# Kernel tuning notes

Measured on AMD Instinct MI355X. Metric: run time of the kernel, lower is better.

Reference implementation:

```python
import jax, jax.numpy as jnp
import numpy as np

B, T, E, D, A, H, C, K = 32, 1500, 512, 512, 512, 4, 10, 201
SHARPENING = 1.0


def setup_inputs() -> dict:
    key = jax.random.key(0)
    ks = jax.random.split(key, 11)
    def w(k, shape, fan_in):
        return jax.random.normal(k, shape, jnp.float32) / np.sqrt(fan_in).astype(np.float32)
    return {
        "enc_out": jax.random.normal(ks[0], (B, T, E), jnp.float32),
        "x_lens": jax.random.randint(ks[1], (B,), T // 2, T + 1),
        "dec_out": jax.random.normal(ks[2], (B, 1, D), jnp.float32),
        # previous-step attention weights: a valid distribution over T per head
        "aw_step": jax.nn.softmax(jax.random.normal(ks[3], (B, T, H), jnp.float32), axis=1),
        "w_enc": w(ks[4], (H, E, A), E),   # per-head LinearND(enc->att)
        "b_enc": jnp.zeros((H, A), jnp.float32),
        "w_dec": w(ks[5], (H, D, A), D),   # per-head LinearND(dec->att), no bias
        "w_conv": w(ks[6], (H, C, A), C),  # per-head LinearND(conv_ch->att), no bias
        "conv_k": w(ks[7], (H * C, 1, K), K),  # grouped 1D conv kernels (O,I,K), groups=H
        "v": w(ks[8], (H, A), A),          # per-head LinearND(att->1), no bias
        "w_mha": w(ks[9], (H * E, E), H * E),
        "b_mha": jnp.zeros((E,), jnp.float32),
    }


def reference(enc_out, x_lens, dec_out, aw_step, w_enc, b_enc, w_dec, w_conv, conv_k, v, w_mha, b_mha):
    b, t, e = enc_out.shape
    h = aw_step.shape[-1]
    c = w_conv.shape[1]
    k = conv_k.shape[-1]
    # enc_out_a: per-head encoder projection [B,T,H,A]
    enc_a = jnp.einsum('bte,hea->btha', enc_out, w_enc) + b_enc
    # decoder projection, broadcast over time [B,1,H,A]
    dec_a = jnp.einsum('bd,hda->bha', dec_out[:, 0], w_dec)[:, None]
    # location features: grouped 1D conv over previous attention weights
    aw_t = jnp.transpose(aw_step, (0, 2, 1))  # [B,H,T]
    conv = jax.lax.conv_general_dilated(
        aw_t, conv_k, window_strides=(1,), padding=[(k // 2, k // 2)],
        dimension_numbers=('NCH', 'OIH', 'NCH'), feature_group_count=h)  # [B,H*C,T]
    conv = conv.reshape(b, h, c, t).transpose(0, 3, 1, 2)  # [B,T,H,C]
    conv_a = jnp.einsum('bthc,hca->btha', conv, w_conv)
    # additive energy [B,T,H]
    energy = jnp.einsum('btha,ha->bth', jnp.tanh(enc_a + dec_a + conv_a), v)
    # original code multiplies energy by mask (1 valid, -1024 padded) then sharpening
    mask = jnp.where(jnp.arange(t)[None, :] < x_lens[:, None], 1.0, -1024.0).astype(energy.dtype)
    energy = energy * mask[:, :, None] * SHARPENING
    aw = jax.nn.softmax(energy, axis=1)  # softmax over time per head
    # per-head context, concatenated along feature dim -> [B,1,H*E]
    ctx = jnp.einsum('bte,bth->bhe', enc_out, aw).reshape(b, 1, h * e)
    ctx = ctx @ w_mha + b_mha  # [B,1,E]
    return ctx, aw
```

## Files before the change

kernel.cpp:

```cpp
#include <hip/hip_runtime.h>
#include <hip/hip_bf16.h>

#define BB 32
#define TT 1500
#define TP 1536
#define EE 512
#define HH 4
#define AA 512
#define NN 2048
#define CC 10
#define KCONV 201
#define KAUG 576

typedef __attribute__((ext_vector_type(8))) __bf16 bf16x8;
typedef __attribute__((ext_vector_type(4))) float f32x4;

__device__ __forceinline__ unsigned short f2bf(float x) {
    unsigned int u = __float_as_uint(x);
    u = (u + 0x7fffu + ((u >> 16) & 1u)) >> 16;
    return (unsigned short)u;
}
__device__ __forceinline__ float bf2f(unsigned short u) {
    return __uint_as_float(((unsigned int)u) << 16);
}
__device__ __forceinline__ void glds16(const void* g, void* l) {
    __builtin_amdgcn_global_load_lds(
        (const __attribute__((address_space(1))) unsigned int*)g,
        (__attribute__((address_space(3))) unsigned int*)l, 16, 0, 0);
}
__device__ __forceinline__ float tanh_fast(float x) {
    float e = __expf(x * 2.0f);
    return fmaf(-2.0f, __builtin_amdgcn_rcpf(e + 1.0f), 1.0f);
}

#define PREP_DEC0   0
#define PREP_CONV0  32
#define PREP_WT0    7712
#define PREP_PAD0   12320
#define PREP_ENC0   19412
#define PREP_TOTAL  43412

__global__ __launch_bounds__(256) void k_prep(
    const float* __restrict__ enc, const int* __restrict__ xl,
    const float* __restrict__ dec_out, const float* __restrict__ aw_step,
    const float* __restrict__ w_enc, const float* __restrict__ b_enc,
    const float* __restrict__ w_dec, const float* __restrict__ w_conv,
    const float* __restrict__ conv_k,
    unsigned short* __restrict__ Whi, unsigned short* __restrict__ Wlo,
    unsigned short* __restrict__ Ahi, unsigned short* __restrict__ Alo,
    float* __restrict__ dec_a) {
    __shared__ float sbuf[456 + KCONV];
    const int bid = blockIdx.x;
    const int tid = threadIdx.x;

    if (bid < PREP_CONV0) {
        const int h = bid >> 3;
        const int a = ((bid & 7) << 6) + (tid & 63);
        const int bg = tid >> 6;
        float acc[8] = {0.f, 0.f, 0.f, 0.f, 0.f, 0.f, 0.f, 0.f};
        const float* wp = w_dec + (size_t)h * 512 * 512 + a;
#pragma unroll 4
        for (int d = 0; d < 512; ++d) {
            float w = wp[(size_t)d * 512];
#pragma unroll
            for (int q = 0; q < 8; ++q)
                acc[q] += dec_out[(size_t)(bg * 8 + q) * 512 + d] * w;
        }
        const float be = b_enc[h * 512 + a];
#pragma unroll
        for (int q = 0; q < 8; ++q)
            dec_a[(size_t)(bg * 8 + q) * NN + h * 512 + a] = be + acc[q];
    } else if (bid < PREP_WT0) {
        int r = bid - PREP_CONV0;
        const int tch = r % 6;
        const int hc  = (r / 6) % 40;
        const int b   = r / 240;
        const int h   = hc / 10;
        const int t0  = tch * 256;
        float* sAw = sbuf;
        float* sK  = sbuf + 456;
        for (int i = tid; i < 456; i += 256) {
            int ts = t0 - 100 + i;
            sAw[i] = (ts >= 0 && ts < TT) ? aw_step[((size_t)b * TT + ts) * HH + h] : 0.f;
        }
        if (tid < KCONV) sK[tid] = conv_k[(size_t)hc * KCONV + tid];
        __syncthreads();
        int t = t0 + tid;
        if (t < TT) {
            float acc = 0.f;
            for (int k = 0; k < KCONV; ++k) acc += sAw[tid + k] * sK[k];
            size_t o = ((size_t)b * TP + t) * KAUG + 512 + hc;
            unsigned short hi = f2bf(acc);
            Ahi[o] = hi; Alo[o] = f2bf(acc - bf2f(hi));
        }
    } else if (bid < PREP_PAD0) {
        int idx = (bid - PREP_WT0) * 256 + tid;
        int n = idx / KAUG, k = idx % KAUG;
        int h = n >> 9, a = n & 511;
        float val = 0.f;
        if (k < 512) {
            val = w_enc[((size_t)h * 512 + k) * 512 + a];
        } else if (k < 552) {
            int j = k - 512; int h2 = j / 10, c = j % 10;
            if (h2 == h) val = w_conv[((size_t)h * 10 + c) * 512 + a];
        }
        unsigned short hi = f2bf(val);
        Whi[idx] = hi;
        Wlo[idx] = f2bf(val - bf2f(hi));
    } else if (bid < PREP_ENC0) {
        int idx = (bid - PREP_PAD0) * 256 + tid;
        const int tot1 = BB * 36 * KAUG;
        const int tot2 = BB * TT * 24;
        size_t o;
        if (idx < tot1) {
            int b = idx / (36 * KAUG); int r2 = idx % (36 * KAUG);
            int t = 1500 + r2 / KAUG;  int k = r2 % KAUG;
            o = ((size_t)b * TP + t) * KAUG + k;
        } else if (idx < tot1 + tot2) {
            int j = idx - tot1;
            int b = j / (TT * 24); int r2 = j % (TT * 24);
            int t = r2 / 24;       int k = 552 + r2 % 24;
            o = ((size_t)b * TP + t) * KAUG + k;
        } else return;
        Ahi[o] = 0; Alo[o] = 0;
    } else {
        long idx = (long)(bid - PREP_ENC0) * 256 + tid;
        if (idx >= 6144000L) return;
        long f = idx * 4;
        int b = (int)(f / 768000);
        int r2 = (int)(f % 768000);
        int t = r2 >> 9, e = r2 & 511;
        float4 vv = *reinterpret_cast<const float4*>(enc + f);
        ushort4 h4;
        h4.x = f2bf(vv.x); h4.y = f2bf(vv.y); h4.z = f2bf(vv.z); h4.w = f2bf(vv.w);
        size_t o = ((size_t)b * TP + t) * KAUG + e;
        *reinterpret_cast<ushort4*>(Ahi + o) = h4;
        if (((t & ~255) + 256) > xl[b]) {
            ushort4 l4;
            l4.x = f2bf(vv.x - bf2f(h4.x));
            l4.y = f2bf(vv.y - bf2f(h4.y));
            l4.z = f2bf(vv.z - bf2f(h4.z));
            l4.w = f2bf(vv.w - bf2f(h4.w));
            *reinterpret_cast<ushort4*>(Alo + o) = l4;
        }
    }
}

__global__ __launch_bounds__(512, 2) void k_gemm(
    const unsigned short* __restrict__ Ahi, const unsigned short* __restrict__ Alo,
    const unsigned short* __restrict__ Whi, const unsigned short* __restrict__ Wlo,
    const float* __restrict__ dec_a, const float* __restrict__ vvec,
    const int* __restrict__ xl, float* __restrict__ energy) {
    __shared__ unsigned short lsA[2][16384];
    __shared__ unsigned short lsB[2][16384];
    const int bid = blockIdx.x;
    const int ntile = bid & 7;
    const int rest = bid >> 3;
    const int b = rest & 31;
    const int mtile = 5 - (rest >> 5);
    const int m0 = mtile * 256, n0 = ntile * 256;
    const int xlen = xl[b];
    const int nkt = (m0 + 256 <= xlen) ? 9 : 27;
    const int nIter = nkt >> 1;

    const int tid = threadIdx.x;
    const int lane = tid & 63, wave = tid >> 6;
    const int wm = wave >> 2, wn = wave & 3;

    f32x4 acc[8][4];
#pragma unroll
    for (int i = 0; i < 8; i++)
#pragma unroll
        for (int j = 0; j < 4; j++) acc[i][j] = (f32x4){0.f, 0.f, 0.f, 0.f};

    const int srow = tid >> 3;
    const int cg8 = ((tid & 7) ^ (srow & 7)) << 3;
    const size_t aRow0 = ((size_t)b * TP + m0 + srow) * KAUG + cg8;
    const size_t bRow0 = ((size_t)n0 + srow) * KAUG + cg8;

    auto stgA = [&](int buf, int half, const unsigned short* Ap, int k0) {
        const unsigned short* s = Ap + aRow0 + (size_t)half * 128 * KAUG + k0;
        unsigned short* d = &lsA[buf][half * 8192 + tid * 8];
        glds16(s, d);
        glds16(s + (size_t)64 * KAUG, d + 4096);
    };
    auto stgB = [&](int buf, int half, const unsigned short* Bp, int k0) {
        const unsigned short* s = Bp + bRow0 + (size_t)half * 128 * KAUG + k0;
        unsigned short* d = &lsB[buf][half * 8192 + tid * 8];
        glds16(s, d);
        glds16(s + (size_t)64 * KAUG, d + 4096);
    };

    const int l15 = lane & 15, lk = lane >> 4, lsw = lane & 7;
    const int aoff = (((wm << 7) + l15) << 6);
    const int boff = (((wn << 6) + l15) << 6);
    const int ac0 = ((lk ^ lsw) << 3);
    const int ac1 = (((4 | lk) ^ lsw) << 3);

    bf16x8 aLo[4][2], aHi[4][2], bLo[2][2], bHi[2][2];

#define RDALO(P) { _Pragma("unroll") for (int i = 0; i < 4; ++i) { \
    aLo[i][0] = *(const bf16x8*)&lsA[P][aoff + i * 1024 + ac0]; \
    aLo[i][1] = *(const bf16x8*)&lsA[P][aoff + i * 1024 + ac1]; } }
#define RDAHI(P) { _Pragma("unroll") for (int i = 0; i < 4; ++i) { \
    aHi[i][0] = *(const bf16x8*)&lsA[P][aoff + (i + 4) * 1024 + ac0]; \
    aHi[i][1] = *(const bf16x8*)&lsA[P][aoff + (i + 4) * 1024 + ac1]; } }
#define RDBLO(P) { _Pragma("unroll") for (int j = 0; j < 2; ++j) { \
    bLo[j][0] = *(const bf16x8*)&lsB[P][boff + j * 1024 + ac0]; \
    bLo[j][1] = *(const bf16x8*)&lsB[P][boff + j * 1024 + ac1]; } }
#define RDBHI(P) { _Pragma("unroll") for (int j = 0; j < 2; ++j) { \
    bHi[j][0] = *(const bf16x8*)&lsB[P][boff + (j + 2) * 1024 + ac0]; \
    bHi[j][1] = *(const bf16x8*)&lsB[P][boff + (j + 2) * 1024 + ac1]; } }
#define MFQ(AARR, IOFF, BARR, JOFF) { \
    _Pragma("unroll") for (int i = 0; i < 4; ++i) \
    _Pragma("unroll") for (int j = 0; j < 2; ++j) { \
        acc[(IOFF) + i][(JOFF) + j] = __builtin_amdgcn_mfma_f32_16x16x32_bf16(AARR[i][0], BARR[j][0], acc[(IOFF) + i][(JOFF) + j], 0, 0, 0); \
        acc[(IOFF) + i][(JOFF) + j] = __builtin_amdgcn_mfma_f32_16x16x32_bf16(AARR[i][1], BARR[j][1], acc[(IOFF) + i][(JOFF) + j], 0, 0, 0); } }
#define PH_ENTER() { __builtin_amdgcn_s_barrier(); \
    asm volatile("s_waitcnt lgkmcnt(0)" ::: "memory"); \
    __builtin_amdgcn_sched_barrier(0); __builtin_amdgcn_s_setprio(1); }
#define PH_EXIT()  { __builtin_amdgcn_s_setprio(0); __builtin_amdgcn_s_barrier(); \
    __builtin_amdgcn_sched_barrier(0); }

    stgA(0, 0, Ahi, 0); stgA(0, 1, Ahi, 0);
    stgB(0, 0, Whi, 0); stgB(0, 1, Whi, 0);
    stgA(1, 0, Ahi, 64); stgA(1, 1, Ahi, 64);
    __builtin_amdgcn_sched_barrier(0);
    asm volatile("s_waitcnt vmcnt(4)" ::: "memory");
    __builtin_amdgcn_s_barrier();
    __builtin_amdgcn_sched_barrier(0);

    for (int it = 0; it < nIter; ++it) {
        const int kt0 = it << 1;
        const int ktA = kt0 + 1, ktB = kt0 + 2, ktC = kt0 + 3;
        const unsigned short* BpA = (ktA >= 9 && ktA < 18) ? Wlo : Whi;
        const int kA = ((ktA >= 18) ? ktA - 18 : (ktA >= 9) ? ktA - 9 : ktA) * 64;
        const unsigned short* ApB = (ktB >= 18) ? Alo : Ahi;
        const unsigned short* BpB = (ktB >= 9 && ktB < 18) ? Wlo : Whi;
        const int kB = ((ktB >= 18) ? ktB - 18 : (ktB >= 9) ? ktB - 9 : ktB) * 64;
        const unsigned short* ApC = (ktC >= 18) ? Alo : Ahi;
        const int kC = ((ktC >= 18) ? ktC - 18 : (ktC >= 9) ? ktC - 9 : ktC) * 64;
        const bool notLast = (it != nIter - 1);

        RDALO(0); RDBLO(0);
        stgB(1, 0, BpA, kA);
        PH_ENTER(); MFQ(aLo, 0, bLo, 0); PH_EXIT();
        RDAHI(0);
        stgB(1, 1, BpA, kA);
        PH_ENTER(); MFQ(aHi, 4, bLo, 0); PH_EXIT();
        RDBHI(0);
        stgA(0, 0, ApB, kB);
        PH_ENTER(); MFQ(aLo, 0, bHi, 2); PH_EXIT();
        stgA(0, 1, ApB, kB);
        __builtin_amdgcn_s_barrier();
        __builtin_amdgcn_sched_barrier(0);
        __builtin_amdgcn_s_setprio(1);
        MFQ(aHi, 4, bHi, 2);
        __builtin_amdgcn_s_setprio(0);
        __builtin_amdgcn_sched_barrier(0);
        asm volatile("s_waitcnt vmcnt(4)" ::: "memory");
        __builtin_amdgcn_s_barrier();
        __builtin_amdgcn_sched_barrier(0);

        RDALO(1); RDBLO(1);
        stgB(0, 0, BpB, kB);
        PH_ENTER(); MFQ(aLo, 0, bLo, 0); PH_EXIT();
        RDAHI(1);
        stgB(0, 1, BpB, kB);
        PH_ENTER(); MFQ(aHi, 4, bLo, 0); PH_EXIT();
        RDBHI(1);
        if (notLast) stgA(1, 0, ApC, kC);
        PH_ENTER(); MFQ(aLo, 0, bHi, 2); PH_EXIT();
        if (notLast) stgA(1, 1, ApC, kC);
        __builtin_amdgcn_s_barrier();
        __builtin_amdgcn_sched_barrier(0);
        __builtin_amdgcn_s_setprio(1);
        MFQ(aHi, 4, bHi, 2);
        __builtin_amdgcn_s_setprio(0);
        __builtin_amdgcn_sched_barrier(0);
        if (notLast) asm volatile("s_waitcnt vmcnt(4)" ::: "memory");
        __builtin_amdgcn_s_barrier();
        __builtin_amdgcn_sched_barrier(0);
    }

    asm volatile("s_waitcnt vmcnt(0)" ::: "memory");
    __builtin_amdgcn_s_barrier();
    __builtin_amdgcn_sched_barrier(0);
    RDALO(0); RDBLO(0);
    asm volatile("s_waitcnt lgkmcnt(0)" ::: "memory");
    __builtin_amdgcn_sched_barrier(0);
    MFQ(aLo, 0, bLo, 0);
    RDAHI(0);
    asm volatile("s_waitcnt lgkmcnt(0)" ::: "memory");
    __builtin_amdgcn_sched_barrier(0);
    MFQ(aHi, 4, bLo, 0);
    RDBHI(0);
    asm volatile("s_waitcnt lgkmcnt(0)" ::: "memory");
    __builtin_amdgcn_sched_barrier(0);
    MFQ(aLo, 0, bHi, 2);
    MFQ(aHi, 4, bHi, 2);
#undef RDALO
#undef RDAHI
#undef RDBLO
#undef RDBHI
#undef MFQ
#undef PH_ENTER
#undef PH_EXIT

    const int h = ntile >> 1;
    const int kg = lane >> 4;
    float dv[4], vv[4];
#pragma unroll
    for (int j = 0; j < 4; j++) {
        int ng = n0 + wn * 64 + j * 16 + (lane & 15);
        dv[j] = dec_a[(size_t)b * NN + ng];
        vv[j] = vvec[ng];
    }
#pragma unroll
    for (int i = 0; i < 8; i++) {
        float part[4] = {0.f, 0.f, 0.f, 0.f};
#pragma unroll
        for (int j = 0; j < 4; j++)
#pragma unroll
            for (int rr = 0; rr < 4; rr++)
                part[rr] += tanh_fast(acc[i][j][rr] + dv[j]) * vv[j];
#pragma unroll
        for (int rr = 0; rr < 4; rr++) {
            float s = part[rr];
            s += __shfl_xor(s, 1, 64);
            s += __shfl_xor(s, 2, 64);
            s += __shfl_xor(s, 4, 64);
            s += __shfl_xor(s, 8, 64);
            if ((lane & 15) == 0) {
                int t = m0 + wm * 128 + i * 16 + kg * 4 + rr;
                if (t < TT)
                    atomicAdd(&energy[((size_t)b * HH + h) * TP + t], s);
            }
        }
    }
}

__global__ __launch_bounds__(512) void k_softmax(const float* __restrict__ energy,
                                                 const int* __restrict__ x_lens,
                                                 float* __restrict__ aw) {
    const int b = blockIdx.x >> 2, h = blockIdx.x & 3;
    const int tid = threadIdx.x;
    __shared__ float sE[TT];
    __shared__ float red[512];
    const int xlen = x_lens[b];
    float lmax = -3.4e38f;
    for (int t = tid; t < TT; t += 512) {
        float e = energy[((size_t)b * HH + h) * TP + t];
        float m = (t < xlen) ? e : e * -1024.0f;
        sE[t] = m;
        lmax = fmaxf(lmax, m);
    }
    red[tid] = lmax; __syncthreads();
    for (int s = 256; s > 0; s >>= 1) { if (tid < s) red[tid] = fmaxf(red[tid], red[tid + s]); __syncthreads(); }
    float mx = red[0]; __syncthreads();
    float lsum = 0.f;
    for (int t = tid; t < TT; t += 512) {
        float ex = expf(sE[t] - mx);
        sE[t] = ex; lsum += ex;
    }
    red[tid] = lsum; __syncthreads();
    for (int s = 256; s > 0; s >>= 1) { if (tid < s) red[tid] += red[tid + s]; __syncthreads(); }
    float sum = red[0];
    for (int t = tid; t < TT; t += 512)
        aw[((size_t)b * TT + t) * HH + h] = sE[t] / sum;
}

__global__ __launch_bounds__(512) void k_ctx(const float* __restrict__ enc,
                                             const float* __restrict__ aw,
                                             float* __restrict__ ctx_h) {
    const int chunk = blockIdx.x, b = blockIdx.y;
    const int t0 = chunk * 64;
    const int nt = (TT - t0 < 64) ? (TT - t0) : 64;
    __shared__ float sA[64 * 4];
    const int tid = threadIdx.x;
    for (int i = tid; i < nt * 4; i += 512)
        sA[i] = aw[((size_t)b * TT + t0) * HH + i];
    __syncthreads();
    float a0 = 0.f, a1 = 0.f, a2 = 0.f, a3 = 0.f;
    const float* ep = enc + ((size_t)b * TT + t0) * EE + tid;
    if (nt == 64) {
#pragma unroll 8
        for (int tt = 0; tt < 64; ++tt) {
            float ev = ep[(size_t)tt * EE];
            a0 += sA[tt * 4 + 0] * ev; a1 += sA[tt * 4 + 1] * ev;
            a2 += sA[tt * 4 + 2] * ev; a3 += sA[tt * 4 + 3] * ev;
        }
    } else {
        for (int tt = 0; tt < nt; ++tt) {
            float ev = ep[(size_t)tt * EE];
            a0 += sA[tt * 4 + 0] * ev; a1 += sA[tt * 4 + 1] * ev;
            a2 += sA[tt * 4 + 2] * ev; a3 += sA[tt * 4 + 3] * ev;
        }
    }
    atomicAdd(&ctx_h[((size_t)b * HH + 0) * EE + tid], a0);
    atomicAdd(&ctx_h[((size_t)b * HH + 1) * EE + tid], a1);
    atomicAdd(&ctx_h[((size_t)b * HH + 2) * EE + tid], a2);
    atomicAdd(&ctx_h[((size_t)b * HH + 3) * EE + tid], a3);
}

__global__ __launch_bounds__(256) void k_mha(const float* __restrict__ ctx_h,
                                             const float* __restrict__ w_mha,
                                             const float* __restrict__ b_mha,
                                             float* __restrict__ out) {
    __shared__ float sred[256];
    const int tid = threadIdx.x;
    const int b  = blockIdx.x >> 2;
    const int eo = ((blockIdx.x & 3) << 7) + (tid & 127);
    const int kg = tid >> 7;
    const float* c = ctx_h + (size_t)b * NN + kg * 1024;
    const float* w = w_mha + ((size_t)kg * 1024) * EE + eo;
    float acc = 0.f;
#pragma unroll 8
    for (int k = 0; k < 1024; ++k) acc += c[k] * w[(size_t)k * EE];
    sred[tid] = acc;
    __syncthreads();
    if (tid < 128)
        out[(size_t)b * EE + eo] = b_mha[eo] + sred[tid] + sred[tid + 128];
}

extern "C" void kernel_launch(void* const* d_in, const int* in_sizes, int n_in,
                              void* d_out, int out_size, void* d_ws, size_t ws_size,
                              hipStream_t stream) {
    (void)in_sizes; (void)n_in; (void)out_size;
    const float* enc    = (const float*)d_in[0];
    const int*   xlen   = (const int*)d_in[1];
    const float* dec    = (const float*)d_in[2];
    const float* aw_in  = (const float*)d_in[3];
    const float* w_enc  = (const float*)d_in[4];
    const float* b_enc  = (const float*)d_in[5];
    const float* w_dec  = (const float*)d_in[6];
    const float* w_conv = (const float*)d_in[7];
    const float* convk  = (const float*)d_in[8];
    const float* v      = (const float*)d_in[9];
    const float* w_mha  = (const float*)d_in[10];
    const float* b_mha  = (const float*)d_in[11];
    float* out = (float*)d_out;

    char* ws = (char*)d_ws;
    unsigned short* Whi = (unsigned short*)ws;
    unsigned short* Wlo = Whi + (size_t)NN * KAUG;
    unsigned short* Ahi = (unsigned short*)(ws + 4718592);
    unsigned short* Alo = Ahi + (size_t)BB * TP * KAUG;
    float* dec_a  = (float*)(ws + 117964800);
    float* energy = (float*)(ws + 118226944);
    float* ctx_h  = (float*)(ws + 119013376);
    (void)ws_size;

    hipMemsetAsync(energy, 0, 786432 + 262144, stream);

    k_prep<<<dim3(PREP_TOTAL), 256, 0, stream>>>(enc, xlen, dec, aw_in, w_enc, b_enc,
                                                 w_dec, w_conv, convk,
                                                 Whi, Wlo, Ahi, Alo, dec_a);
    k_gemm<<<dim3(1536), 512, 0, stream>>>(Ahi, Alo, Whi, Wlo, dec_a, v, xlen, energy);
    k_softmax<<<dim3(BB * HH), 512, 0, stream>>>(energy, xlen, out + 16384);
    k_ctx <<<dim3(24, BB), 512, 0, stream>>>(enc, out + 16384, ctx_h);
    k_mha <<<dim3(128), 256, 0, stream>>>(ctx_h, w_mha, b_mha, out);
}
```

Measured before the change: 581.8 us.

## Drop explicit waitcnt and sched barriers in GEMM loop; shrink pad-zeroing prep

Removes the manual lgkmcnt(0) waits and sched_barrier fences around the MFMA phases, so the compiler can interleave LDS reads with MFMAs and insert finer-grained waits. It also stops zeroing the padded time rows (t>=1500) in the prep kernel and zeroes only the 24 pad columns per row using vectorized ushort4 stores, which cuts the prep block count. The risk is that the pad rows are no longer zeroed, which is unsafe if later code reads them, and that compiler scheduling may break the hand-tuned ping-pong phases.

```diff
diff --git a/kernel.cpp b/kernel.cpp
--- a/kernel.cpp
+++ b/kernel.cpp
@@ -36,9 +36,9 @@
 #define PREP_DEC0   0
 #define PREP_CONV0  32
 #define PREP_WT0    7712
-#define PREP_PAD0   12320
-#define PREP_ENC0   19412
-#define PREP_TOTAL  43412
+#define PREP_PADC0  12320
+#define PREP_ENC0   13445
+#define PREP_TOTAL  37445
 
 __global__ __launch_bounds__(256) void k_prep(
     const float* __restrict__ enc, const int* __restrict__ xl,
@@ -93,7 +93,7 @@
             unsigned short hi = f2bf(acc);
             Ahi[o] = hi; Alo[o] = f2bf(acc - bf2f(hi));
         }
-    } else if (bid < PREP_PAD0) {
+    } else if (bid < PREP_PADC0) {
         int idx = (bid - PREP_WT0) * 256 + tid;
         int n = idx / KAUG, k = idx % KAUG;
         int h = n >> 9, a = n & 511;
@@ -108,21 +108,15 @@
         Whi[idx] = hi;
         Wlo[idx] = f2bf(val - bf2f(hi));
     } else if (bid < PREP_ENC0) {
-        int idx = (bid - PREP_PAD0) * 256 + tid;
-        const int tot1 = BB * 36 * KAUG;
-        const int tot2 = BB * TT * 24;
-        size_t o;
-        if (idx < tot1) {
-            int b = idx / (36 * KAUG); int r2 = idx % (36 * KAUG);
-            int t = 1500 + r2 / KAUG;  int k = r2 % KAUG;
-            o = ((size_t)b * TP + t) * KAUG + k;
-        } else if (idx < tot1 + tot2) {
-            int j = idx - tot1;
-            int b = j / (TT * 24); int r2 = j % (TT * 24);
-            int t = r2 / 24;       int k = 552 + r2 % 24;
-            o = ((size_t)b * TP + t) * KAUG + k;
-        } else return;
-        Ahi[o] = 0; Alo[o] = 0;
+        int idx = (bid - PREP_PADC0) * 256 + tid;
+        if (idx >= BB * TT * 6) return;
+        int u = idx % 6;
+        int row = idx / 6;
+        int b = row / TT, t = row % TT;
+        size_t o = ((size_t)b * TP + t) * KAUG + 552 + u * 4;
+        ushort4 z = {0, 0, 0, 0};
+        *reinterpret_cast<ushort4*>(Ahi + o) = z;
+        *reinterpret_cast<ushort4*>(Alo + o) = z;
     } else {
         long idx = (long)(bid - PREP_ENC0) * 256 + tid;
         if (idx >= 6144000L) return;
@@ -216,11 +210,8 @@
     _Pragma("unroll") for (int j = 0; j < 2; ++j) { \
         acc[(IOFF) + i][(JOFF) + j] = __builtin_amdgcn_mfma_f32_16x16x32_bf16(AARR[i][0], BARR[j][0], acc[(IOFF) + i][(JOFF) + j], 0, 0, 0); \
         acc[(IOFF) + i][(JOFF) + j] = __builtin_amdgcn_mfma_f32_16x16x32_bf16(AARR[i][1], BARR[j][1], acc[(IOFF) + i][(JOFF) + j], 0, 0, 0); } }
-#define PH_ENTER() { __builtin_amdgcn_s_barrier(); \
-    asm volatile("s_waitcnt lgkmcnt(0)" ::: "memory"); \
-    __builtin_amdgcn_sched_barrier(0); __builtin_amdgcn_s_setprio(1); }
-#define PH_EXIT()  { __builtin_amdgcn_s_setprio(0); __builtin_amdgcn_s_barrier(); \
-    __builtin_amdgcn_sched_barrier(0); }
+#define PH_ENTER() { __builtin_amdgcn_s_barrier(); __builtin_amdgcn_s_setprio(1); }
+#define PH_EXIT()  { __builtin_amdgcn_s_setprio(0); __builtin_amdgcn_s_barrier(); }
 
     stgA(0, 0, Ahi, 0); stgA(0, 1, Ahi, 0);
     stgB(0, 0, Whi, 0); stgB(0, 1, Whi, 0);
@@ -253,7 +244,6 @@
         PH_ENTER(); MFQ(aLo, 0, bHi, 2); PH_EXIT();
         stgA(0, 1, ApB, kB);
         __builtin_amdgcn_s_barrier();
-        __builtin_amdgcn_sched_barrier(0);
         __builtin_amdgcn_s_setprio(1);
         MFQ(aHi, 4, bHi, 2);
         __builtin_amdgcn_s_setprio(0);
@@ -273,7 +263,6 @@
         PH_ENTER(); MFQ(aLo, 0, bHi, 2); PH_EXIT();
         if (notLast) stgA(1, 1, ApC, kC);
         __builtin_amdgcn_s_barrier();
-        __builtin_amdgcn_sched_barrier(0);
         __builtin_amdgcn_s_setprio(1);
         MFQ(aHi, 4, bHi, 2);
         __builtin_amdgcn_s_setprio(0);
@@ -287,16 +276,10 @@
     __builtin_amdgcn_s_barrier();
     __builtin_amdgcn_sched_barrier(0);
     RDALO(0); RDBLO(0);
-    asm volatile("s_waitcnt lgkmcnt(0)" ::: "memory");
-    __builtin_amdgcn_sched_barrier(0);
     MFQ(aLo, 0, bLo, 0);
     RDAHI(0);
-    asm volatile("s_waitcnt lgkmcnt(0)" ::: "memory");
-    __builtin_amdgcn_sched_barrier(0);
     MFQ(aHi, 4, bLo, 0);
     RDBHI(0);
-    asm volatile("s_waitcnt lgkmcnt(0)" ::: "memory");
-    __builtin_amdgcn_sched_barrier(0);
     MFQ(aLo, 0, bHi, 2);
     MFQ(aHi, 4, bHi, 2);
 #undef RDALO
```

New measurement: 580.6 us. Within noise of the previous version (-0.2%).
